# Kernel optimization log

Hardware: AMD Instinct MI355X
Metric: run time of the kernel (lower is better)

Reference implementation:

```python
import jax, jax.numpy as jnp
import numpy as np

B, S, E, D = 8, 4096, 16, 128   # batch, seq_len, n_experts, d_head
G = S // E                       # tokens routed to each expert


def setup_inputs() -> dict:
    key = jax.random.key(0)
    k1, k2, k3, k4 = jax.random.split(key, 4)
    Q = jax.random.normal(k1, (B, S, D), jnp.float32)
    K = jax.random.normal(k2, (B, S, D), jnp.float32)
    V = jax.random.normal(k3, (B, S, D), jnp.float32)
    # balanced hard routing: random permutation -> exactly G tokens per expert
    perm = jax.vmap(lambda k: jax.random.permutation(k, S))(jax.random.split(k4, B))  # [B,S]
    expert_ids = jnp.repeat(jnp.arange(E, dtype=jnp.int32), G)  # [S]
    assign = jnp.zeros((B, S), jnp.int32).at[jnp.arange(B)[:, None], perm].set(expert_ids[None, :])
    route_mat = jax.nn.one_hot(assign, E, dtype=jnp.float32)  # [B,S,E]
    # causal mask within each expert block; True = masked (filled with -inf)
    mask = jnp.triu(jnp.ones((G, G), dtype=bool), k=1)
    return {"Q": Q, "K": K, "V": V, "route_mat": route_mat, "mask": mask}


def reference(Q, K, V, route_mat, mask):
    # RowParallelMatmulWithMoE: gather each expert's routed tokens, block QK^T
    assign = jnp.argmax(route_mat, axis=-1)                 # [B,S]
    order = jnp.argsort(assign, axis=-1, stable=True)       # group tokens by expert
    idx = order.reshape(B, E, G)                            # [B,E,G]
    gather = jax.vmap(lambda x, i: x[i])                    # per-batch gather
    Qe, Ke, Ve = gather(Q, idx), gather(K, idx), gather(V, idx)  # [B,E,G,D]
    scores = jnp.einsum('begd,behd->begh', Qe, Ke)          # [B,E,G,G]
    dot = scores / jnp.sqrt(jnp.float32(D))
    m = mask[:G, :G]
    dot = jnp.where(m[None, None, :, :], -jnp.inf, dot)
    attn = jax.nn.softmax(dot, axis=-1)                     # dropout p=0.0 -> identity
    # ColumnParallelMatmulWithMoE, combine_head=False: per-expert AV
    X = jnp.einsum('begh,behd->begd', attn, Ve)             # [B,E,G,D]
    return X
```

## Files before the change

kernel.cpp:

```cpp
#include <hip/hip_runtime.h>
#include <hip/hip_bf16.h>

#define NB 8
#define NS 4096
#define NE 16
#define ND 128
#define NG 256

typedef float  f32x4 __attribute__((ext_vector_type(4)));
typedef short  s16x8 __attribute__((ext_vector_type(8)));
typedef short  s16x4 __attribute__((ext_vector_type(4)));

#define SCALE_LOG2E 0.12752749570528832f
#define NEGF (-1e30f)

__device__ __forceinline__ short f2bf(float f) {
  unsigned u = __builtin_bit_cast(unsigned, f);
  unsigned r = (u + 0x7fffu + ((u >> 16) & 1u)) >> 16;
  return (short)r;
}

__global__ __launch_bounds__(256) void gather_kernel(const float* __restrict__ RM,
                                                     int* __restrict__ idx_out) {
  __shared__ int cnt[256];
  const int tid = threadIdx.x;
  const int be = blockIdx.x;
  const int b = be >> 4;
  const int e = be & 15;
  const float* rmb = RM + (size_t)b * NS * NE + e;
  unsigned mbits = 0;
  int cloc = 0;
  #pragma unroll
  for (int i = 0; i < 16; ++i) {
    bool m = rmb[(size_t)(tid * 16 + i) * NE] > 0.5f;
    mbits |= (m ? 1u : 0u) << i;
    cloc += m ? 1 : 0;
  }
  cnt[tid] = cloc;
  __syncthreads();
  for (int off = 1; off < 256; off <<= 1) {
    int v = cnt[tid];
    int add = (tid >= off) ? cnt[tid - off] : 0;
    __syncthreads();
    cnt[tid] = v + add;
    __syncthreads();
  }
  int pos = cnt[tid] - cloc;
  int* ob = idx_out + (size_t)be * NG;
  for (int i = 0; i < 16; ++i)
    if (mbits & (1u << i)) ob[pos++] = tid * 16 + i;
}

__global__ __launch_bounds__(256, 2) void sattn_kernel(
    const float* __restrict__ Qg, const float* __restrict__ Kg,
    const float* __restrict__ Vg, const int* __restrict__ IdxW,
    float* __restrict__ Out) {
  __shared__ int idx[NG];
  __shared__ __align__(16) short kv[NG * ND];
  __shared__ __align__(16) short plds[4][16 * 64];

  const int tid = threadIdx.x;
  const int lane = tid & 63;
  const int w = tid >> 6;
  const int c15 = lane & 15;
  const int hi = lane >> 4;

  const int bid = blockIdx.x;
  const int be = bid >> 2;
  const int j = bid & 3;
  const int b = be >> 4;

  const int RT = (w == 0) ? j : (w == 1) ? (7 - j) : (w == 2) ? (8 + j) : (15 - j);
  const int R = (16 - j) * 16;

  idx[tid] = IdxW[(size_t)be * NG + tid];
  __syncthreads();

  s16x8 qf[4];
  {
    const int g = RT * 16 + c15;
    const float* qrow = Qg + ((size_t)b * NS + idx[g]) * ND;
    #pragma unroll
    for (int kb = 0; kb < 4; ++kb) {
      const int d0 = kb * 32 + hi * 8;
      float4 x = *(const float4*)(qrow + d0);
      float4 y = *(const float4*)(qrow + d0 + 4);
      s16x8 q;
      q[0] = f2bf(x.x); q[1] = f2bf(x.y); q[2] = f2bf(x.z); q[3] = f2bf(x.w);
      q[4] = f2bf(y.x); q[5] = f2bf(y.y); q[6] = f2bf(y.z); q[7] = f2bf(y.w);
      qf[kb] = q;
    }
  }

  {
    const int row_off = tid >> 5;
    const int c4 = tid & 31;
    const float* kbase = Kg + (size_t)b * NS * ND;
    #pragma unroll 4
    for (int r0 = 0; r0 < R; r0 += 8) {
      int h = r0 + row_off;
      int tok = idx[h];
      float4 v = *(const float4*)(kbase + (size_t)tok * ND + c4 * 4);
      s16x4 p;
      p[0] = f2bf(v.x); p[1] = f2bf(v.y); p[2] = f2bf(v.z); p[3] = f2bf(v.w);
      int byte = h * 256 + ((c4 * 8) ^ ((h & 7) << 4));
      *(s16x4*)((char*)kv + byte) = p;
    }
  }
  __syncthreads();

  f32x4 s[16];
  #pragma unroll
  for (int ct = 0; ct < 16; ++ct) {
    f32x4 acc = f32x4{0.f, 0.f, 0.f, 0.f};
    if (ct <= RT) {
      #pragma unroll
      for (int kb = 0; kb < 4; ++kb) {
        int h = ct * 16 + c15;
        int byte = h * 256 + (((kb * 32 + hi * 8) * 2) ^ ((h & 7) << 4));
        s16x8 kf = *(const s16x8*)((const char*)kv + byte);
        acc = __builtin_amdgcn_mfma_f32_16x16x32_bf16(qf[kb], kf, acc, 0, 0, 0);
      }
      if (ct == RT) {
        #pragma unroll
        for (int r = 0; r < 4; ++r)
          if (c15 > hi * 4 + r) acc[r] = NEGF;
      }
    } else {
      acc = f32x4{NEGF, NEGF, NEGF, NEGF};
    }
    s[ct] = acc;
  }

  #pragma unroll
  for (int r = 0; r < 4; ++r) {
    float m = NEGF;
    #pragma unroll
    for (int ct = 0; ct < 16; ++ct) m = fmaxf(m, s[ct][r]);
    m = fmaxf(m, __shfl_xor(m, 1));
    m = fmaxf(m, __shfl_xor(m, 2));
    m = fmaxf(m, __shfl_xor(m, 4));
    m = fmaxf(m, __shfl_xor(m, 8));
    float sum = 0.f;
    #pragma unroll
    for (int ct = 0; ct < 16; ++ct) {
      float p = exp2f((s[ct][r] - m) * SCALE_LOG2E);
      s[ct][r] = p;
      sum += p;
    }
    sum += __shfl_xor(sum, 1);
    sum += __shfl_xor(sum, 2);
    sum += __shfl_xor(sum, 4);
    sum += __shfl_xor(sum, 8);
    float rinv = 1.0f / sum;
    #pragma unroll
    for (int ct = 0; ct < 16; ++ct) s[ct][r] *= rinv;
  }

  __syncthreads();

  {
    const int row = tid;
    const float* vrow = Vg + ((size_t)b * NS + idx[row]) * ND;
    #pragma unroll 4
    for (int p4 = 0; p4 < 32; ++p4) {
      float4 v = *(const float4*)(vrow + p4 * 4);
      #pragma unroll
      for (int i = 0; i < 4; ++i) {
        int d = p4 * 4 + i;
        float val = (i == 0) ? v.x : (i == 1) ? v.y : (i == 2) ? v.z : v.w;
        int byte = d * 512 + ((row * 2) ^ ((d & 7) << 4));
        *(short*)((char*)kv + byte) = f2bf(val);
      }
    }
  }
  __syncthreads();

  char* plw = (char*)plds[w];
  f32x4 o[8];
  #pragma unroll
  for (int dt = 0; dt < 8; ++dt) o[dt] = f32x4{0.f, 0.f, 0.f, 0.f};

  #pragma unroll
  for (int hc = 0; hc < 4; ++hc) {
    if (hc * 4 <= RT) {
      #pragma unroll
      for (int cr = 0; cr < 4; ++cr) {
        const int ct = hc * 4 + cr;
        #pragma unroll
        for (int r = 0; r < 4; ++r) {
          int gl = hi * 4 + r;
          int byte = gl * 128 + (((cr * 16 + c15) * 2) ^ ((gl & 7) << 4));
          *(short*)(plw + byte) = f2bf(s[ct][r]);
        }
      }
      #pragma unroll
      for (int kb = 0; kb < 2; ++kb) {
        int abyte = c15 * 128 + (((kb * 32 + hi * 8) * 2) ^ ((c15 & 7) << 4));
        s16x8 pf = *(const s16x8*)(plw + abyte);
        #pragma unroll
        for (int dt = 0; dt < 8; ++dt) {
          int d = dt * 16 + c15;
          int hof = hc * 64 + kb * 32 + hi * 8;
          int vbyte = d * 512 + ((hof * 2) ^ ((d & 7) << 4));
          s16x8 vf = *(const s16x8*)((const char*)kv + vbyte);
          o[dt] = __builtin_amdgcn_mfma_f32_16x16x32_bf16(pf, vf, o[dt], 0, 0, 0);
        }
      }
    }
  }

  float* outbase = Out + ((size_t)be * NG + RT * 16) * ND;
  #pragma unroll
  for (int dt = 0; dt < 8; ++dt) {
    #pragma unroll
    for (int r = 0; r < 4; ++r)
      outbase[(size_t)(hi * 4 + r) * ND + dt * 16 + c15] = o[dt][r];
  }
}

extern "C" void kernel_launch(void* const* d_in, const int* in_sizes, int n_in,
                              void* d_out, int out_size, void* d_ws, size_t ws_size,
                              hipStream_t stream) {
  const float* Q  = (const float*)d_in[0];
  const float* K  = (const float*)d_in[1];
  const float* V  = (const float*)d_in[2];
  const float* RM = (const float*)d_in[3];
  float* Out = (float*)d_out;
  int* idx_ws = (int*)d_ws;

  gather_kernel<<<dim3(NB * NE), dim3(256), 0, stream>>>(RM, idx_ws);
  sattn_kernel<<<dim3(NB * NE * 4), dim3(256), 0, stream>>>(Q, K, V, idx_ws, Out);
}
```

Before: 121.1 us.

## Fuse routing-index scan into attention kernel and prefetch V into registers

Removes the separate gather kernel launch: each attention block now recomputes its expert's token index list from the routing matrix with an in-LDS prefix scan, reusing the kv buffer as scratch. V rows are loaded into registers (converted to bf16) early, so the global V latency overlaps the QK^T and softmax phases. Each of the four blocks per expert now redundantly scans the routing matrix. Holding 32 packed V vectors per thread raises register pressure, which may cause spills or lower occupancy under the 2-blocks launch bound.

Result: slower. 130.6 us (+7.9%).

```diff
diff --git a/kernel.cpp b/kernel.cpp
--- a/kernel.cpp
+++ b/kernel.cpp
@@ -20,40 +20,80 @@
   return (short)r;
 }
 
-__global__ __launch_bounds__(256) void gather_kernel(const float* __restrict__ RM,
-                                                     int* __restrict__ idx_out) {
-  __shared__ int cnt[256];
-  const int tid = threadIdx.x;
-  const int be = blockIdx.x;
-  const int b = be >> 4;
-  const int e = be & 15;
-  const float* rmb = RM + (size_t)b * NS * NE + e;
-  unsigned mbits = 0;
-  int cloc = 0;
-  #pragma unroll
-  for (int i = 0; i < 16; ++i) {
-    bool m = rmb[(size_t)(tid * 16 + i) * NE] > 0.5f;
-    mbits |= (m ? 1u : 0u) << i;
-    cloc += m ? 1 : 0;
-  }
-  cnt[tid] = cloc;
-  __syncthreads();
-  for (int off = 1; off < 256; off <<= 1) {
-    int v = cnt[tid];
-    int add = (tid >= off) ? cnt[tid - off] : 0;
-    __syncthreads();
-    cnt[tid] = v + add;
-    __syncthreads();
-  }
-  int pos = cnt[tid] - cloc;
-  int* ob = idx_out + (size_t)be * NG;
-  for (int i = 0; i < 16; ++i)
-    if (mbits & (1u << i)) ob[pos++] = tid * 16 + i;
+__device__ __forceinline__ void softmax_norm16(f32x4 (&s)[16]) {
+  #pragma unroll
+  for (int r = 0; r < 4; ++r) {
+    float m = NEGF;
+    #pragma unroll
+    for (int ct = 0; ct < 16; ++ct) m = fmaxf(m, s[ct][r]);
+    m = fmaxf(m, __shfl_xor(m, 1));
+    m = fmaxf(m, __shfl_xor(m, 2));
+    m = fmaxf(m, __shfl_xor(m, 4));
+    m = fmaxf(m, __shfl_xor(m, 8));
+    float sum = 0.f;
+    #pragma unroll
+    for (int ct = 0; ct < 16; ++ct) {
+      float p = exp2f((s[ct][r] - m) * SCALE_LOG2E);
+      s[ct][r] = p;
+      sum += p;
+    }
+    sum += __shfl_xor(sum, 1);
+    sum += __shfl_xor(sum, 2);
+    sum += __shfl_xor(sum, 4);
+    sum += __shfl_xor(sum, 8);
+    float rinv = 1.0f / sum;
+    #pragma unroll
+    for (int ct = 0; ct < 16; ++ct) s[ct][r] *= rinv;
+  }
+}
+
+__device__ __forceinline__ void pv_store16(const f32x4 (&s)[16], int RT,
+                                           const char* kvb, char* plw,
+                                           float* outbase, int c15, int hi) {
+  f32x4 o[8];
+  #pragma unroll
+  for (int dt = 0; dt < 8; ++dt) o[dt] = f32x4{0.f, 0.f, 0.f, 0.f};
+
+  #pragma unroll
+  for (int hc = 0; hc < 4; ++hc) {
+    if (hc * 4 <= RT) {
+      #pragma unroll
+      for (int cr = 0; cr < 4; ++cr) {
+        const int ct = hc * 4 + cr;
+        #pragma unroll
+        for (int r = 0; r < 4; ++r) {
+          float pv = (ct <= RT) ? s[ct][r] : 0.0f;
+          int gl = hi * 4 + r;
+          int byte = gl * 128 + (((cr * 16 + c15) * 2) ^ ((gl & 7) << 4));
+          *(short*)(plw + byte) = f2bf(pv);
+        }
+      }
+      #pragma unroll
+      for (int kb = 0; kb < 2; ++kb) {
+        int abyte = c15 * 128 + (((kb * 32 + hi * 8) * 2) ^ ((c15 & 7) << 4));
+        s16x8 pf = *(const s16x8*)(plw + abyte);
+        #pragma unroll
+        for (int dt = 0; dt < 8; ++dt) {
+          int d = dt * 16 + c15;
+          int hof = hc * 64 + kb * 32 + hi * 8;
+          int vbyte = d * 512 + ((hof * 2) ^ ((d & 7) << 4));
+          s16x8 vf = *(const s16x8*)(kvb + vbyte);
+          o[dt] = __builtin_amdgcn_mfma_f32_16x16x32_bf16(pf, vf, o[dt], 0, 0, 0);
+        }
+      }
+    }
+  }
+  #pragma unroll
+  for (int dt = 0; dt < 8; ++dt) {
+    #pragma unroll
+    for (int r = 0; r < 4; ++r)
+      outbase[(size_t)(hi * 4 + r) * ND + dt * 16 + c15] = o[dt][r];
+  }
 }
 
 __global__ __launch_bounds__(256, 2) void sattn_kernel(
     const float* __restrict__ Qg, const float* __restrict__ Kg,
-    const float* __restrict__ Vg, const int* __restrict__ IdxW,
+    const float* __restrict__ Vg, const float* __restrict__ RM,
     float* __restrict__ Out) {
   __shared__ int idx[NG];
   __shared__ __align__(16) short kv[NG * ND];
@@ -69,17 +109,51 @@
   const int be = bid >> 2;
   const int j = bid & 3;
   const int b = be >> 4;
+  const int e = be & 15;
 
   const int RT = (w == 0) ? j : (w == 1) ? (7 - j) : (w == 2) ? (8 + j) : (15 - j);
   const int R = (16 - j) * 16;
 
-  idx[tid] = IdxW[(size_t)be * NG + tid];
-  __syncthreads();
+  {
+    int* cnt = (int*)kv;
+    const float* rmb = RM + (size_t)b * NS * NE + e;
+    unsigned mbits = 0;
+    int cloc = 0;
+    #pragma unroll
+    for (int i = 0; i < 16; ++i) {
+      bool m = rmb[(size_t)(tid * 16 + i) * NE] > 0.5f;
+      mbits |= (m ? 1u : 0u) << i;
+      cloc += m ? 1 : 0;
+    }
+    cnt[tid] = cloc;
+    __syncthreads();
+    for (int off = 1; off < 256; off <<= 1) {
+      int v = cnt[tid];
+      int add = (tid >= off) ? cnt[tid - off] : 0;
+      __syncthreads();
+      cnt[tid] = v + add;
+      __syncthreads();
+    }
+    int pos = cnt[tid] - cloc;
+    for (int i = 0; i < 16; ++i)
+      if (mbits & (1u << i)) idx[pos++] = tid * 16 + i;
+    __syncthreads();
+  }
+
+  s16x4 vreg[32];
+  {
+    const float* vrow = Vg + ((size_t)b * NS + idx[tid]) * ND;
+    #pragma unroll
+    for (int p4 = 0; p4 < 32; ++p4) {
+      float4 v = *(const float4*)(vrow + p4 * 4);
+      vreg[p4][0] = f2bf(v.x); vreg[p4][1] = f2bf(v.y);
+      vreg[p4][2] = f2bf(v.z); vreg[p4][3] = f2bf(v.w);
+    }
+  }
 
   s16x8 qf[4];
   {
-    const int g = RT * 16 + c15;
-    const float* qrow = Qg + ((size_t)b * NS + idx[g]) * ND;
+    const float* qrow = Qg + ((size_t)b * NS + idx[RT * 16 + c15]) * ND;
     #pragma unroll
     for (int kb = 0; kb < 4; ++kb) {
       const int d0 = kb * 32 + hi * 8;
@@ -96,7 +170,6 @@
     const int row_off = tid >> 5;
     const int c4 = tid & 31;
     const float* kbase = Kg + (size_t)b * NS * ND;
-    #pragma unroll 4
     for (int r0 = 0; r0 < R; r0 += 8) {
       int h = r0 + row_off;
       int tok = idx[h];
@@ -132,91 +205,27 @@
     s[ct] = acc;
   }
 
-  #pragma unroll
-  for (int r = 0; r < 4; ++r) {
-    float m = NEGF;
-    #pragma unroll
-    for (int ct = 0; ct < 16; ++ct) m = fmaxf(m, s[ct][r]);
-    m = fmaxf(m, __shfl_xor(m, 1));
-    m = fmaxf(m, __shfl_xor(m, 2));
-    m = fmaxf(m, __shfl_xor(m, 4));
-    m = fmaxf(m, __shfl_xor(m, 8));
-    float sum = 0.f;
-    #pragma unroll
-    for (int ct = 0; ct < 16; ++ct) {
-      float p = exp2f((s[ct][r] - m) * SCALE_LOG2E);
-      s[ct][r] = p;
-      sum += p;
-    }
-    sum += __shfl_xor(sum, 1);
-    sum += __shfl_xor(sum, 2);
-    sum += __shfl_xor(sum, 4);
-    sum += __shfl_xor(sum, 8);
-    float rinv = 1.0f / sum;
-    #pragma unroll
-    for (int ct = 0; ct < 16; ++ct) s[ct][r] *= rinv;
-  }
+  softmax_norm16(s);
 
   __syncthreads();
 
   {
     const int row = tid;
-    const float* vrow = Vg + ((size_t)b * NS + idx[row]) * ND;
-    #pragma unroll 4
+    #pragma unroll
     for (int p4 = 0; p4 < 32; ++p4) {
-      float4 v = *(const float4*)(vrow + p4 * 4);
       #pragma unroll
       for (int i = 0; i < 4; ++i) {
         int d = p4 * 4 + i;
-        float val = (i == 0) ? v.x : (i == 1) ? v.y : (i == 2) ? v.z : v.w;
         int byte = d * 512 + ((row * 2) ^ ((d & 7) << 4));
-        *(short*)((char*)kv + byte) = f2bf(val);
+        *(short*)((char*)kv + byte) = vreg[p4][i];
       }
     }
   }
   __syncthreads();
 
   char* plw = (char*)plds[w];
-  f32x4 o[8];
-  #pragma unroll
-  for (int dt = 0; dt < 8; ++dt) o[dt] = f32x4{0.f, 0.f, 0.f, 0.f};
-
-  #pragma unroll
-  for (int hc = 0; hc < 4; ++hc) {
-    if (hc * 4 <= RT) {
-      #pragma unroll
-      for (int cr = 0; cr < 4; ++cr) {
-        const int ct = hc * 4 + cr;
-        #pragma unroll
-        for (int r = 0; r < 4; ++r) {
-          int gl = hi * 4 + r;
-          int byte = gl * 128 + (((cr * 16 + c15) * 2) ^ ((gl & 7) << 4));
-          *(short*)(plw + byte) = f2bf(s[ct][r]);
-        }
-      }
-      #pragma unroll
-      for (int kb = 0; kb < 2; ++kb) {
-        int abyte = c15 * 128 + (((kb * 32 + hi * 8) * 2) ^ ((c15 & 7) << 4));
-        s16x8 pf = *(const s16x8*)(plw + abyte);
-        #pragma unroll
-        for (int dt = 0; dt < 8; ++dt) {
-          int d = dt * 16 + c15;
-          int hof = hc * 64 + kb * 32 + hi * 8;
-          int vbyte = d * 512 + ((hof * 2) ^ ((d & 7) << 4));
-          s16x8 vf = *(const s16x8*)((const char*)kv + vbyte);
-          o[dt] = __builtin_amdgcn_mfma_f32_16x16x32_bf16(pf, vf, o[dt], 0, 0, 0);
-        }
-      }
-    }
-  }
-
-  float* outbase = Out + ((size_t)be * NG + RT * 16) * ND;
-  #pragma unroll
-  for (int dt = 0; dt < 8; ++dt) {
-    #pragma unroll
-    for (int r = 0; r < 4; ++r)
-      outbase[(size_t)(hi * 4 + r) * ND + dt * 16 + c15] = o[dt][r];
-  }
+  float* ob = Out + ((size_t)be * NG + RT * 16) * ND;
+  pv_store16(s, RT, (const char*)kv, plw, ob, c15, hi);
 }
 
 extern "C" void kernel_launch(void* const* d_in, const int* in_sizes, int n_in,
@@ -227,8 +236,5 @@
   const float* V  = (const float*)d_in[2];
   const float* RM = (const float*)d_in[3];
   float* Out = (float*)d_out;
-  int* idx_ws = (int*)d_ws;
-
-  gather_kernel<<<dim3(NB * NE), dim3(256), 0, stream>>>(RM, idx_ws);
-  sattn_kernel<<<dim3(NB * NE * 4), dim3(256), 0, stream>>>(Q, K, V, idx_ws, Out);
-}
+  sattn_kernel<<<dim3(NB * NE * 4), dim3(256), 0, stream>>>(Q, K, V, RM, Out);
+}
```
